# Optimization experiments

Measured on AMD Instinct MI355X. Metric: run time of the kernel, lower is better.

Reference implementation:

```python
import jax, jax.numpy as jnp
import numpy as np

B, P, S, D = 16, 512, 1024, 1024
H_FULL, H_LIGHT = 16, 8


def _mha(q, k, v, w_in, b_in, w_out, b_out, nh):
    # PyTorch nn.MultiheadAttention (batch_first=True), dropout=0 (eval).
    d = q.shape[-1]
    hd = d // nh
    wq, wk, wv = jnp.split(w_in, 3, axis=0)
    bq, bk, bv = jnp.split(b_in, 3, axis=0)

    def proj(x, w, b):
        return (x @ w.T + b).reshape(x.shape[0], x.shape[1], nh, hd)

    qh = proj(q, wq, bq)  # [B,Lq,H,hd]
    kh = proj(k, wk, bk)  # [B,Lk,H,hd]
    vh = proj(v, wv, bv)
    scale = 1.0 / jnp.sqrt(jnp.asarray(hd, q.dtype))
    scores = jnp.einsum('bqhd,bkhd->bhqk', qh, kh) * scale
    attn = jax.nn.softmax(scores, axis=-1)
    o = jnp.einsum('bhqk,bkhd->bqhd', attn, vh).reshape(q.shape[0], q.shape[1], d)
    out = o @ w_out.T + b_out
    return out, attn.mean(axis=1)  # avg weights over heads (torch default)


def _ln(x, g, b, eps=1e-5):
    mu = x.mean(-1, keepdims=True)
    var = ((x - mu) ** 2).mean(-1, keepdims=True)
    return (x - mu) / jnp.sqrt(var + eps) * g + b


def setup_inputs() -> dict:
    key = jax.random.key(0)
    ks = jax.random.split(key, 16)
    w = 0.02
    inp = {
        'proto': jax.random.normal(ks[0], (B, P, D), jnp.float32),
        'img_features': jax.random.normal(ks[1], (B, S, D), jnp.float32),
        'cross_w_in': jax.random.normal(ks[2], (3 * D, D), jnp.float32) * w,
        'cross_b_in': jnp.zeros((3 * D,), jnp.float32),
        'cross_w_out': jax.random.normal(ks[3], (D, D), jnp.float32) * w,
        'cross_b_out': jnp.zeros((D,), jnp.float32),
        'self_w_in': jax.random.normal(ks[4], (3 * D, D), jnp.float32) * w,
        'self_b_in': jnp.zeros((3 * D,), jnp.float32),
        'self_w_out': jax.random.normal(ks[5], (D, D), jnp.float32) * w,
        'self_b_out': jnp.zeros((D,), jnp.float32),
        'light_w_in': jax.random.normal(ks[6], (3 * D, D), jnp.float32) * w,
        'light_b_in': jnp.zeros((3 * D,), jnp.float32),
        'light_w_out': jax.random.normal(ks[7], (D, D), jnp.float32) * w,
        'light_b_out': jnp.zeros((D,), jnp.float32),
        'norm1_g': jnp.ones((D,), jnp.float32), 'norm1_b': jnp.zeros((D,), jnp.float32),
        'norm2_g': jnp.ones((D,), jnp.float32), 'norm2_b': jnp.zeros((D,), jnp.float32),
        'norm3_g': jnp.ones((D,), jnp.float32), 'norm3_b': jnp.zeros((D,), jnp.float32),
        'gate_w1': jax.random.normal(ks[8], (D, 3 * D), jnp.float32) * w,
        'gate_b1': jnp.zeros((D,), jnp.float32),
        'gate_w2': jax.random.normal(ks[9], (3, D), jnp.float32) * w,
        'gate_b2': jnp.zeros((3,), jnp.float32),
    }
    return inp


def reference(proto, img_features,
              cross_w_in, cross_b_in, cross_w_out, cross_b_out,
              self_w_in, self_b_in, self_w_out, self_b_out,
              light_w_in, light_b_in, light_w_out, light_b_out,
              norm1_g, norm1_b, norm2_g, norm2_b, norm3_g, norm3_b,
              gate_w1, gate_b1, gate_w2, gate_b2):
    cross_raw, attn_w = _mha(proto, img_features, img_features,
                             cross_w_in, cross_b_in, cross_w_out, cross_b_out, H_FULL)
    cross_out = _ln(proto + cross_raw, norm1_g, norm1_b)
    self_raw, _ = _mha(cross_out, cross_out, cross_out,
                       self_w_in, self_b_in, self_w_out, self_b_out, H_FULL)
    self_out = _ln(cross_out + self_raw, norm2_g, norm2_b)
    light_raw, _ = _mha(self_out, self_out, self_out,
                        light_w_in, light_b_in, light_w_out, light_b_out, H_LIGHT)
    light_out = _ln(self_out + light_raw, norm3_g, norm3_b)
    gate_in = jnp.concatenate([cross_out, self_out, light_out], axis=-1)  # [B,P,3D]
    h = jax.nn.gelu(gate_in @ gate_w1.T + gate_b1, approximate=False)
    gate_w = jax.nn.softmax(h @ gate_w2.T + gate_b2, axis=-1)  # [B,P,3]
    updated = (gate_w[..., 0:1] * cross_out
               + gate_w[..., 1:2] * self_out
               + gate_w[..., 2:3] * light_out)
    return updated, attn_w
```

## Files before the change

### kernel.cpp

```cpp
#include <hip/hip_runtime.h>
#include <hip/hip_bf16.h>

typedef __hip_bfloat16 bf16;
typedef __attribute__((ext_vector_type(8))) short short8;
typedef __attribute__((ext_vector_type(4))) float f32x4;

#define BD 16
#define PD 512
#define SD 1024
#define DD 1024

#define GLDS16(gp, lp)                                              \
  __builtin_amdgcn_global_load_lds(                                 \
      (const __attribute__((address_space(1))) void*)(gp),          \
      (__attribute__((address_space(3))) void*)(lp), 16, 0, 0)

__global__ __launch_bounds__(256) void f2b(const float* __restrict__ in,
                                           bf16* __restrict__ out, int n)
{
  int i = (blockIdx.x * 256 + threadIdx.x) * 4;
  if (i < n) {
    float4 v = *(const float4*)(in + i);
    out[i + 0] = __float2bfloat16(v.x);
    out[i + 1] = __float2bfloat16(v.y);
    out[i + 2] = __float2bfloat16(v.z);
    out[i + 3] = __float2bfloat16(v.w);
  }
}

__global__ __launch_bounds__(256) void gemm_nt(
    const bf16* __restrict__ A, int lda,
    const bf16* __restrict__ W, int ldw,
    const float* __restrict__ bias,
    bf16* __restrict__ C, int ldc,
    int K, int gelu)
{
  __shared__ bf16 As[3][128 * 32];
  __shared__ bf16 Bs[3][128 * 32];

  const int t = threadIdx.x;
  const int lane = t & 63, wv = t >> 6;
  const int m0 = blockIdx.y * 128;
  const int n0 = blockIdx.x * 128;
  const int rl = lane & 15, qd = lane >> 4;

  f32x4 acc[4][4];
  for (int i = 0; i < 4; i++)
    for (int j = 0; j < 4; j++)
      acc[i][j] = (f32x4){0.f, 0.f, 0.f, 0.f};

  const int scol = ((t & 3) ^ ((t >> 2) & 3)) * 8;
  const bf16* Ag = A + (size_t)(m0 + (t >> 2)) * lda + scol;
  const bf16* Wg = W + (size_t)(n0 + (t >> 2)) * ldw + scol;
  const size_t a_half = (size_t)64 * lda, w_half = (size_t)64 * ldw;
  const int lo = wv * 512;

  const int mw = (wv >> 1) * 64, nw = (wv & 1) * 64;
  const int slo = rl & 3;

  const int nt = K >> 5;

#define STAGE(buf, k0)                          \
  do {                                          \
    GLDS16(Ag + (k0), &As[buf][lo]);            \
    GLDS16(Ag + a_half + (k0), &As[buf][2048 + lo]); \
    GLDS16(Wg + (k0), &Bs[buf][lo]);            \
    GLDS16(Wg + w_half + (k0), &Bs[buf][2048 + lo]); \
  } while (0)

  STAGE(0, 0);
  STAGE(1, 32);

  int cur = 0, pf = 2;
  for (int tt = 0; tt < nt; ++tt) {
    if (tt + 1 < nt) asm volatile("s_waitcnt vmcnt(4)" ::: "memory");
    else             asm volatile("s_waitcnt vmcnt(0)" ::: "memory");
    __builtin_amdgcn_s_barrier();
    if (tt + 2 < nt) STAGE(pf, (tt + 2) * 32);

    const bf16* Ac = As[cur];
    const bf16* Bc = Bs[cur];
    short8 a[4], b[4];
#pragma unroll
    for (int i = 0; i < 4; i++)
      a[i] = *(const short8*)&Ac[(mw + i * 16 + rl) * 32 + (qd ^ slo) * 8];
#pragma unroll
    for (int j = 0; j < 4; j++)
      b[j] = *(const short8*)&Bc[(nw + j * 16 + rl) * 32 + (qd ^ slo) * 8];
#pragma unroll
    for (int i = 0; i < 4; i++)
#pragma unroll
      for (int j = 0; j < 4; j++)
        acc[i][j] = __builtin_amdgcn_mfma_f32_16x16x32_bf16(a[i], b[j], acc[i][j], 0, 0, 0);

    cur = (cur == 2) ? 0 : cur + 1;
    pf  = (pf == 2) ? 0 : pf + 1;
  }
#undef STAGE

  for (int i = 0; i < 4; i++) {
    const int row = m0 + mw + i * 16 + qd * 4;
    for (int j = 0; j < 4; j++) {
      const int col = n0 + nw + j * 16 + rl;
      const float bv = bias[col];
      for (int r = 0; r < 4; r++) {
        float v = acc[i][j][r] + bv;
        if (gelu) v = 0.5f * v * (1.0f + erff(v * 0.70710678118654752f));
        C[(size_t)(row + r) * ldc + col] = __float2bfloat16(v);
      }
    }
  }
}

__global__ __launch_bounds__(512, 2) void gemm_nt256(
    const bf16* __restrict__ A, int lda,
    const bf16* __restrict__ W, int ldw,
    const float* __restrict__ bias,
    bf16* __restrict__ C, int ldc,
    int K, int gelu)
{
  __shared__ bf16 As[2][256 * 64];
  __shared__ bf16 Bs[2][256 * 64];

  const int t = threadIdx.x;
  const int lane = t & 63, wv = t >> 6;
  const int rl = lane & 15, qd = lane >> 4;
  const int m0 = blockIdx.y * 256;
  const int n0 = blockIdx.x * 256;
  const int mw = (wv >> 2) * 128, nw = (wv & 3) * 64;

  f32x4 acc[8][4];
#pragma unroll
  for (int i = 0; i < 8; i++)
#pragma unroll
    for (int j = 0; j < 4; j++)
      acc[i][j] = (f32x4){0.f, 0.f, 0.f, 0.f};

  const int scol = ((t & 7) ^ ((t >> 3) & 7)) * 8;
  const bf16* Ag = A + (size_t)(m0 + (t >> 3)) * lda + scol;
  const bf16* Wg = W + (size_t)(n0 + (t >> 3)) * ldw + scol;

#define STAGE256(buf, k0)                                              \
  do {                                                                 \
    _Pragma("unroll")                                                  \
    for (int s = 0; s < 4; s++) {                                      \
      GLDS16(Ag + (size_t)(s * 64) * lda + (k0), &As[buf][s * 4096 + wv * 512]); \
      GLDS16(Wg + (size_t)(s * 64) * ldw + (k0), &Bs[buf][s * 4096 + wv * 512]); \
    }                                                                  \
  } while (0)

  const int nt = K >> 6;
  const int slo = rl & 7;

  STAGE256(0, 0);

  for (int tt = 0; tt < nt; ++tt) {
    if (tt + 1 < nt) {
      STAGE256((tt + 1) & 1, (tt + 1) * 64);
      asm volatile("s_waitcnt vmcnt(8)" ::: "memory");
    } else {
      asm volatile("s_waitcnt vmcnt(0)" ::: "memory");
    }
    __builtin_amdgcn_s_barrier();

    const bf16* Ac = As[tt & 1];
    const bf16* Bc = Bs[tt & 1];
#pragma unroll
    for (int kk = 0; kk < 2; ++kk) {
      const int cs = ((kk * 4 + qd) ^ slo) * 8;
      short8 a[8], b[4];
#pragma unroll
      for (int i = 0; i < 8; i++)
        a[i] = *(const short8*)&Ac[(mw + i * 16 + rl) * 64 + cs];
#pragma unroll
      for (int j = 0; j < 4; j++)
        b[j] = *(const short8*)&Bc[(nw + j * 16 + rl) * 64 + cs];
#pragma unroll
      for (int i = 0; i < 8; i++)
#pragma unroll
        for (int j = 0; j < 4; j++)
          acc[i][j] = __builtin_amdgcn_mfma_f32_16x16x32_bf16(a[i], b[j], acc[i][j], 0, 0, 0);
    }
    __builtin_amdgcn_s_barrier();
  }
#undef STAGE256

  for (int i = 0; i < 8; i++) {
    const int row = m0 + mw + i * 16 + qd * 4;
    for (int j = 0; j < 4; j++) {
      const int col = n0 + nw + j * 16 + rl;
      const float bv = bias[col];
      for (int r = 0; r < 4; r++) {
        float v = acc[i][j][r] + bv;
        if (gelu) v = 0.5f * v * (1.0f + erff(v * 0.70710678118654752f));
        C[(size_t)(row + r) * ldc + col] = __float2bfloat16(v);
      }
    }
  }
}

__global__ void transpose_v(const bf16* __restrict__ V, int ldv, int voff,
                            bf16* __restrict__ Vt, int L, int H, int hd)
{
  __shared__ float tile[32][33];
  const int bh = blockIdx.z;
  const int b = bh / H, h = bh % H;
  const int d0 = blockIdx.x * 32, s0 = blockIdx.y * 32;
  const int tx = threadIdx.x, ty = threadIdx.y;
  tile[ty][tx] = __bfloat162float(V[(size_t)(b * L + s0 + ty) * ldv + voff + h * hd + d0 + tx]);
  __syncthreads();
  Vt[(size_t)((b * H + h) * hd + d0 + ty) * L + s0 + tx] = __float2bfloat16(tile[tx][ty]);
}

template<int HD, bool STATS>
__global__ __launch_bounds__(256) void flash_attn(
    const bf16* __restrict__ Q, int ldq, int qoff,
    const bf16* __restrict__ Km, int ldk, int koff,
    const bf16* __restrict__ Vt,
    bf16* __restrict__ O, int ldo, int ooff,
    float* __restrict__ linv_out,
    int H, int Lq, int Lk, float scale)
{
  constexpr int KK = HD / 32;
  constexpr int NO = HD / 16;
  __shared__ __align__(16) __hip_bfloat16 pl[4][2][2][16][32];

  const int lane = threadIdx.x & 63, wv = threadIdx.x >> 6;
  const int rl = lane & 15, qd = lane >> 4;
  const int b = blockIdx.z, h = blockIdx.y;
  const int q0 = blockIdx.x * 128 + wv * 32;

  short8 qf[2][KK];
  for (int mt = 0; mt < 2; ++mt)
    for (int kk = 0; kk < KK; ++kk)
      qf[mt][kk] = *(const short8*)(Q + (size_t)(b * Lq + q0 + mt * 16 + rl) * ldq
                                      + qoff + h * HD + kk * 32 + qd * 8);

  const bf16* Kb = Km + (size_t)b * Lk * ldk + koff + h * HD + qd * 8;
  const bf16* Vb = Vt + (size_t)(b * H + h) * HD * Lk + qd * 8;

  float ls[2][4];
  for (int mt = 0; mt < 2; mt++)
    for (int r = 0; r < 4; r++) ls[mt][r] = 0.f;
  f32x4 oacc[2][NO];
  for (int mt = 0; mt < 2; mt++)
    for (int ni = 0; ni < NO; ni++) oacc[mt][ni] = (f32x4){0.f, 0.f, 0.f, 0.f};

  const int nS32 = Lk / 32;
  for (int i = 0; i < nS32; i++) {
    const int s0 = i * 32;
    for (int f = 0; f < 2; f++) {
      short8 kf[KK];
#pragma unroll
      for (int kk = 0; kk < KK; kk++)
        kf[kk] = *(const short8*)(Kb + (size_t)(s0 + f * 16 + rl) * ldk + kk * 32);
#pragma unroll
      for (int mt = 0; mt < 2; mt++) {
        f32x4 sc = (f32x4){0.f, 0.f, 0.f, 0.f};
#pragma unroll
        for (int kk = 0; kk < KK; kk++)
          sc = __builtin_amdgcn_mfma_f32_16x16x32_bf16(qf[mt][kk], kf[kk], sc, 0, 0, 0);
        for (int r = 0; r < 4; r++) {
          float p = __expf(sc[r] * scale);
          ls[mt][r] += p;
          pl[wv][i & 1][mt][qd * 4 + r][f * 16 + rl] = __float2bfloat16(p);
        }
      }
    }
    asm volatile("s_waitcnt lgkmcnt(0)" ::: "memory");
    short8 vf[NO];
#pragma unroll
    for (int ni = 0; ni < NO; ni++)
      vf[ni] = *(const short8*)(Vb + (size_t)(ni * 16 + rl) * Lk + s0);
#pragma unroll
    for (int mt = 0; mt < 2; mt++) {
      short8 pa = *(const short8*)&pl[wv][i & 1][mt][rl][qd * 8];
#pragma unroll
      for (int ni = 0; ni < NO; ni++)
        oacc[mt][ni] = __builtin_amdgcn_mfma_f32_16x16x32_bf16(pa, vf[ni], oacc[mt][ni], 0, 0, 0);
    }
  }

  float rinv[2][4];
  for (int mt = 0; mt < 2; mt++)
    for (int r = 0; r < 4; r++) {
      float v = ls[mt][r];
      for (int o = 1; o < 16; o <<= 1) v += __shfl_xor(v, o);
      rinv[mt][r] = 1.0f / v;
    }

  if (STATS) {
    if (rl == 0)
      for (int mt = 0; mt < 2; mt++)
        for (int r = 0; r < 4; r++)
          linv_out[((size_t)b * H + h) * Lq + q0 + mt * 16 + qd * 4 + r] = rinv[mt][r];
  }

  for (int mt = 0; mt < 2; mt++)
    for (int ni = 0; ni < NO; ni++)
      for (int r = 0; r < 4; r++)
        O[(size_t)(b * Lq + q0 + mt * 16 + qd * 4 + r) * ldo + ooff + h * HD + ni * 16 + rl]
            = __float2bfloat16(oacc[mt][ni][r] * rinv[mt][r]);
}

template<int HD>
__global__ __launch_bounds__(256) void probs_mean(
    const bf16* __restrict__ Q, int ldq, int qoff,
    const bf16* __restrict__ Km, int ldk, int koff,
    const float* __restrict__ linv, float* __restrict__ out_att,
    int H, int Lq, int Lk, float scale)
{
  constexpr int KK = HD / 32;
  const int lane = threadIdx.x & 63, wv = threadIdx.x >> 6;
  const int rl = lane & 15, qd = lane >> 4;
  const int b = blockIdx.z;
  const int q0 = blockIdx.x * 128 + wv * 32;
  const int s0 = blockIdx.y * 32;
  const float hs = 1.0f / 16.0f;

  f32x4 am[2][2];
  for (int mt = 0; mt < 2; mt++)
    for (int f = 0; f < 2; f++) am[mt][f] = (f32x4){0.f, 0.f, 0.f, 0.f};

  const bf16* Qb  = Q  + (size_t)(b * Lq + q0) * ldq + qoff + qd * 8;
  const bf16* Kb0 = Km + (size_t)(b * Lk + s0) * ldk + koff + qd * 8;
  const float* lb = linv + (size_t)b * H * Lq + q0 + qd * 4;

  for (int h = 0; h < H; h++) {
    short8 qf[2][KK], kf[2][KK];
#pragma unroll
    for (int mt = 0; mt < 2; mt++)
#pragma unroll
      for (int kk = 0; kk < KK; kk++)
        qf[mt][kk] = *(const short8*)(Qb + (size_t)(mt * 16 + rl) * ldq + h * HD + kk * 32);
#pragma unroll
    for (int f = 0; f < 2; f++)
#pragma unroll
      for (int kk = 0; kk < KK; kk++)
        kf[f][kk] = *(const short8*)(Kb0 + (size_t)(f * 16 + rl) * ldk + h * HD + kk * 32);
    float li[2][4];
#pragma unroll
    for (int mt = 0; mt < 2; mt++)
#pragma unroll
      for (int r = 0; r < 4; r++)
        li[mt][r] = lb[(size_t)h * Lq + mt * 16 + r];
#pragma unroll
    for (int mt = 0; mt < 2; mt++)
#pragma unroll
      for (int f = 0; f < 2; f++) {
        f32x4 sc = (f32x4){0.f, 0.f, 0.f, 0.f};
#pragma unroll
        for (int kk = 0; kk < KK; kk++)
          sc = __builtin_amdgcn_mfma_f32_16x16x32_bf16(qf[mt][kk], kf[f][kk], sc, 0, 0, 0);
#pragma unroll
        for (int r = 0; r < 4; r++)
          am[mt][f][r] += __expf(sc[r] * scale) * li[mt][r];
      }
  }

#pragma unroll
  for (int mt = 0; mt < 2; mt++)
#pragma unroll
    for (int f = 0; f < 2; f++)
#pragma unroll
      for (int r = 0; r < 4; r++)
        out_att[(size_t)(b * Lq + q0 + mt * 16 + qd * 4 + r) * Lk + s0 + f * 16 + rl]
            = am[mt][f][r] * hs;
}

template<bool XF32>
__global__ __launch_bounds__(256) void add_ln(
    const void* __restrict__ Xv, int ldx, int xoff,
    const bf16* __restrict__ Y,
    const float* __restrict__ g, const float* __restrict__ bb,
    bf16* __restrict__ out, int ldo, int ooff)
{
  const int row = blockIdx.x, t = threadIdx.x;
  const bf16* yr = Y + (size_t)row * 1024;
  float v[4], s = 0.f, s2 = 0.f;
  for (int i = 0; i < 4; i++) {
    int c = t * 4 + i;
    float xv;
    if (XF32) xv = ((const float*)Xv)[(size_t)row * ldx + xoff + c];
    else      xv = __bfloat162float(((const bf16*)Xv)[(size_t)row * ldx + xoff + c]);
    v[i] = xv + __bfloat162float(yr[c]);
    s += v[i]; s2 += v[i] * v[i];
  }
  __shared__ float red[2][4];
  for (int o = 32; o >= 1; o >>= 1) { s += __shfl_down(s, o); s2 += __shfl_down(s2, o); }
  const int wv = t >> 6, lane = t & 63;
  if (lane == 0) { red[0][wv] = s; red[1][wv] = s2; }
  __syncthreads();
  s  = red[0][0] + red[0][1] + red[0][2] + red[0][3];
  s2 = red[1][0] + red[1][1] + red[1][2] + red[1][3];
  const float mean = s * (1.0f / 1024.f);
  const float var = s2 * (1.0f / 1024.f) - mean * mean;
  const float rstd = rsqrtf(var + 1e-5f);
  for (int i = 0; i < 4; i++) {
    int c = t * 4 + i;
    float o = (v[i] - mean) * rstd * g[c] + bb[c];
    out[(size_t)row * ldo + ooff + c] = __float2bfloat16(o);
  }
}

__global__ __launch_bounds__(256) void gate_kernel(
    const bf16* __restrict__ Hb, const bf16* __restrict__ G,
    const float* __restrict__ w2, const float* __restrict__ b2,
    float* __restrict__ out)
{
  const int row = blockIdx.x, t = threadIdx.x;
  const bf16* hr = Hb + (size_t)row * 1024;
  float d0 = 0.f, d1 = 0.f, d2 = 0.f;
  for (int i = 0; i < 4; i++) {
    int c = t * 4 + i;
    float hv = __bfloat162float(hr[c]);
    d0 += hv * w2[c];
    d1 += hv * w2[1024 + c];
    d2 += hv * w2[2048 + c];
  }
  __shared__ float red[3][4];
  for (int o = 32; o >= 1; o >>= 1) {
    d0 += __shfl_down(d0, o); d1 += __shfl_down(d1, o); d2 += __shfl_down(d2, o);
  }
  const int wv = t >> 6, lane = t & 63;
  if (lane == 0) { red[0][wv] = d0; red[1][wv] = d1; red[2][wv] = d2; }
  __syncthreads();
  float l0 = red[0][0] + red[0][1] + red[0][2] + red[0][3] + b2[0];
  float l1 = red[1][0] + red[1][1] + red[1][2] + red[1][3] + b2[1];
  float l2 = red[2][0] + red[2][1] + red[2][2] + red[2][3] + b2[2];
  float mm = fmaxf(l0, fmaxf(l1, l2));
  float e0 = __expf(l0 - mm), e1 = __expf(l1 - mm), e2 = __expf(l2 - mm);
  float inv = 1.f / (e0 + e1 + e2);
  float g0 = e0 * inv, g1 = e1 * inv, g2 = e2 * inv;
  const bf16* gr = G + (size_t)row * 3072;
  for (int i = 0; i < 4; i++) {
    int c = t * 4 + i;
    float o = g0 * __bfloat162float(gr[c]) + g1 * __bfloat162float(gr[1024 + c])
            + g2 * __bfloat162float(gr[2048 + c]);
    out[(size_t)row * 1024 + c] = o;
  }
}

extern "C" void kernel_launch(void* const* d_in, const int* in_sizes, int n_in,
                              void* d_out, int out_size, void* d_ws, size_t ws_size,
                              hipStream_t stream)
{
  const float* proto = (const float*)d_in[0];
  const float* img   = (const float*)d_in[1];
  const float* c_wi  = (const float*)d_in[2];
  const float* c_bi  = (const float*)d_in[3];
  const float* c_wo  = (const float*)d_in[4];
  const float* c_bo  = (const float*)d_in[5];
  const float* s_wi  = (const float*)d_in[6];
  const float* s_bi  = (const float*)d_in[7];
  const float* s_wo  = (const float*)d_in[8];
  const float* s_bo  = (const float*)d_in[9];
  const float* l_wi  = (const float*)d_in[10];
  const float* l_bi  = (const float*)d_in[11];
  const float* l_wo  = (const float*)d_in[12];
  const float* l_bo  = (const float*)d_in[13];
  const float* n1g = (const float*)d_in[14]; const float* n1b = (const float*)d_in[15];
  const float* n2g = (const float*)d_in[16]; const float* n2b = (const float*)d_in[17];
  const float* n3g = (const float*)d_in[18]; const float* n3b = (const float*)d_in[19];
  const float* gw1 = (const float*)d_in[20]; const float* gb1 = (const float*)d_in[21];
  const float* gw2 = (const float*)d_in[22]; const float* gb2 = (const float*)d_in[23];

  float* out_upd = (float*)d_out;
  float* out_att = out_upd + (size_t)BD * PD * DD;

  char* ws = (char*)d_ws;
  bf16* WB = (bf16*)ws;
  bf16* w_cwi = WB + 0;
  bf16* w_cwo = WB + 3145728;
  bf16* w_swi = WB + 4194304;
  bf16* w_swo = WB + 7340032;
  bf16* w_lwi = WB + 8388608;
  bf16* w_lwo = WB + 11534336;
  bf16* w_gw1 = WB + 12582912;

  int bc = 16;
  while (bc > 1 && 31457280ull + (size_t)bc * 16777216ull > ws_size) bc >>= 1;

  char* pool = ws + 31457280;
  bf16*  Pb    = (bf16*)pool;
  bf16*  Ib    = (bf16*)(pool + (size_t)1048576 * bc);
  bf16*  G     = (bf16*)(pool + (size_t)3145728 * bc);
  bf16*  KVb   = (bf16*)(pool + (size_t)6291456 * bc);
  bf16*  Bq    = (bf16*)(pool + (size_t)8388608 * bc);
  bf16*  Vt    = (bf16*)(pool + (size_t)11534336 * bc);
  bf16*  Qc    = (bf16*)(pool + (size_t)13631488 * bc);
  bf16*  AO    = (bf16*)(pool + (size_t)14680064 * bc);
  bf16*  OP    = (bf16*)(pool + (size_t)15728640 * bc);
  float* linvb = (float*)(pool + (size_t)15728640 * bc);

  const dim3 blk(256);
  const dim3 blk512(512);

  f2b<<<dim3(3072), blk, 0, stream>>>(c_wi, w_cwi, 3145728);
  f2b<<<dim3(1024), blk, 0, stream>>>(c_wo, w_cwo, 1048576);
  f2b<<<dim3(3072), blk, 0, stream>>>(s_wi, w_swi, 3145728);
  f2b<<<dim3(1024), blk, 0, stream>>>(s_wo, w_swo, 1048576);
  f2b<<<dim3(3072), blk, 0, stream>>>(l_wi, w_lwi, 3145728);
  f2b<<<dim3(1024), blk, 0, stream>>>(l_wo, w_lwo, 1048576);
  f2b<<<dim3(3072), blk, 0, stream>>>(gw1, w_gw1, 3145728);

  for (int b0 = 0; b0 < BD; b0 += bc) {
    const float* proto_c = proto + (size_t)b0 * PD * DD;
    const float* img_c   = img + (size_t)b0 * SD * DD;
    float* out_upd_c = out_upd + (size_t)b0 * PD * DD;
    float* out_att_c = out_att + (size_t)b0 * PD * SD;
    const int MP = bc * PD;
    const int MS = bc * SD;

    f2b<<<dim3(MP), blk, 0, stream>>>(proto_c, Pb, MP * DD);
    f2b<<<dim3(MS), blk, 0, stream>>>(img_c, Ib, MS * DD);

    gemm_nt<<<dim3(8, MP / 128), blk, 0, stream>>>(Pb, 1024, w_cwi, 1024, c_bi,
                                                   Qc, 1024, 1024, 0);
    gemm_nt256<<<dim3(8, MS / 256), blk512, 0, stream>>>(
        Ib, 1024, w_cwi + (size_t)1024 * 1024, 1024, c_bi + 1024, KVb, 2048, 1024, 0);
    transpose_v<<<dim3(2, 32, bc * 16), dim3(32, 32), 0, stream>>>(KVb, 2048, 1024, Vt, 1024, 16, 64);
    flash_attn<64, true><<<dim3(4, 16, bc), blk, 0, stream>>>(
        Qc, 1024, 0, KVb, 2048, 0, Vt, AO, 1024, 0, linvb, 16, PD, SD, 0.125f);
    probs_mean<64><<<dim3(4, SD / 32, bc), blk, 0, stream>>>(
        Qc, 1024, 0, KVb, 2048, 0, linvb, out_att_c, 16, PD, SD, 0.125f);
    gemm_nt<<<dim3(8, MP / 128), blk, 0, stream>>>(AO, 1024, w_cwo, 1024, c_bo, OP, 1024, 1024, 0);
    add_ln<true><<<dim3(MP), blk, 0, stream>>>(proto_c, 1024, 0, OP, n1g, n1b, G, 3072, 0);

    gemm_nt256<<<dim3(12, MP / 256), blk512, 0, stream>>>(
        G, 3072, w_swi, 1024, s_bi, Bq, 3072, 1024, 0);
    transpose_v<<<dim3(2, 16, bc * 16), dim3(32, 32), 0, stream>>>(Bq, 3072, 2048, Vt, 512, 16, 64);
    flash_attn<64, false><<<dim3(4, 16, bc), blk, 0, stream>>>(
        Bq, 3072, 0, Bq, 3072, 1024, Vt, AO, 1024, 0, nullptr, 16, PD, PD, 0.125f);
    gemm_nt<<<dim3(8, MP / 128), blk, 0, stream>>>(AO, 1024, w_swo, 1024, s_bo, OP, 1024, 1024, 0);
    add_ln<false><<<dim3(MP), blk, 0, stream>>>(G, 3072, 0, OP, n2g, n2b, G, 3072, 1024);

    gemm_nt256<<<dim3(12, MP / 256), blk512, 0, stream>>>(
        G + 1024, 3072, w_lwi, 1024, l_bi, Bq, 3072, 1024, 0);
    transpose_v<<<dim3(4, 16, bc * 8), dim3(32, 32), 0, stream>>>(Bq, 3072, 2048, Vt, 512, 8, 128);
    flash_attn<128, false><<<dim3(4, 8, bc), blk, 0, stream>>>(
        Bq, 3072, 0, Bq, 3072, 1024, Vt, AO, 1024, 0, nullptr, 8, PD, PD,
        0.08838834764831845f);
    gemm_nt<<<dim3(8, MP / 128), blk, 0, stream>>>(AO, 1024, w_lwo, 1024, l_bo, OP, 1024, 1024, 0);
    add_ln<false><<<dim3(MP), blk, 0, stream>>>(G, 3072, 1024, OP, n3g, n3b, G, 3072, 2048);

    gemm_nt256<<<dim3(4, MP / 256), blk512, 0, stream>>>(
        G, 3072, w_gw1, 3072, gb1, Qc, 1024, 3072, 1);
    gate_kernel<<<dim3(MP), blk, 0, stream>>>(Qc, G, gw2, gb2, out_upd_c);
  }
}
```

Before: 1.507 ms.

## Split 256-tile GEMM into four interleaved load/MFMA phases per K step

```diff
diff --git a/kernel.cpp b/kernel.cpp
--- a/kernel.cpp
+++ b/kernel.cpp
@@ -112,7 +112,7 @@
   }
 }
 
-__global__ __launch_bounds__(512, 2) void gemm_nt256(
+__global__ __launch_bounds__(512, 2) void gemm8p(
     const bf16* __restrict__ A, int lda,
     const bf16* __restrict__ W, int ldw,
     const float* __restrict__ bias,
@@ -125,66 +125,78 @@
   const int t = threadIdx.x;
   const int lane = t & 63, wv = t >> 6;
   const int rl = lane & 15, qd = lane >> 4;
-  const int m0 = blockIdx.y * 256;
-  const int n0 = blockIdx.x * 256;
+  const int m0 = blockIdx.y * 256, n0 = blockIdx.x * 256;
+  const int aw = (wv >> 2) * 64;
+  const int bw = (wv & 3) * 32;
+  const int slo = rl & 7;
+
+  f32x4 acc[8][4];
+#pragma unroll
+  for (int i = 0; i < 8; i++)
+#pragma unroll
+    for (int j = 0; j < 4; j++) acc[i][j] = (f32x4){0.f, 0.f, 0.f, 0.f};
+
+  const int lr = lane >> 3;
+  const int scol = ((lane & 7) ^ lr) * 8;
+  const bf16* Ag = A + (size_t)(m0 + wv * 8 + lr) * lda + scol;
+  const bf16* Wg = W + (size_t)(n0 + (wv >> 2) * 64 + (wv & 3) * 8 + lr) * ldw + scol;
+  const int ldsw = wv * 512;
+
+#define ST_ALO(bf_, k0_) { GLDS16(Ag + (k0_), &As[bf_][ldsw]);                     \
+                           GLDS16(Ag + (size_t)128 * lda + (k0_), &As[bf_][4096 + ldsw]); }
+#define ST_AHI(bf_, k0_) { GLDS16(Ag + (size_t)64 * lda + (k0_), &As[bf_][8192 + ldsw]); \
+                           GLDS16(Ag + (size_t)192 * lda + (k0_), &As[bf_][12288 + ldsw]); }
+#define ST_BLO(bf_, k0_) { GLDS16(Wg + (k0_), &Bs[bf_][ldsw]);                     \
+                           GLDS16(Wg + (size_t)128 * ldw + (k0_), &Bs[bf_][4096 + ldsw]); }
+#define ST_BHI(bf_, k0_) { GLDS16(Wg + (size_t)32 * ldw + (k0_), &Bs[bf_][8192 + ldsw]); \
+                           GLDS16(Wg + (size_t)160 * ldw + (k0_), &Bs[bf_][12288 + ldsw]); }
+
+#define PHASE(rb_, mh_, nh_, STG)                                                   \
+  {                                                                                 \
+    short8 a0[4][2], b0[2][2];                                                      \
+    const bf16* Ab_ = &As[rb_][(size_t)((mh_) * 128 + aw) * 64];                    \
+    const bf16* Bb_ = &Bs[rb_][(size_t)((nh_) * 128 + bw) * 64];                    \
+    _Pragma("unroll") for (int i2 = 0; i2 < 4; i2++)                                \
+      _Pragma("unroll") for (int kk = 0; kk < 2; kk++)                              \
+        a0[i2][kk] = *(const short8*)&Ab_[(i2 * 16 + rl) * 64 + ((kk * 4 + qd) ^ slo) * 8]; \
+    _Pragma("unroll") for (int j2 = 0; j2 < 2; j2++)                                \
+      _Pragma("unroll") for (int kk = 0; kk < 2; kk++)                              \
+        b0[j2][kk] = *(const short8*)&Bb_[(j2 * 16 + rl) * 64 + ((kk * 4 + qd) ^ slo) * 8]; \
+    STG;                                                                            \
+    asm volatile("s_waitcnt vmcnt(4)" ::: "memory");                                \
+    __builtin_amdgcn_s_barrier();                                                   \
+    __builtin_amdgcn_s_setprio(1);                                                  \
+    _Pragma("unroll") for (int i2 = 0; i2 < 4; i2++)                                \
+      _Pragma("unroll") for (int j2 = 0; j2 < 2; j2++)                              \
+        _Pragma("unroll") for (int kk = 0; kk < 2; kk++)                            \
+          acc[(mh_) * 4 + i2][(nh_) * 2 + j2] = __builtin_amdgcn_mfma_f32_16x16x32_bf16( \
+              a0[i2][kk], b0[j2][kk], acc[(mh_) * 4 + i2][(nh_) * 2 + j2], 0, 0, 0); \
+    __builtin_amdgcn_s_setprio(0);                                                  \
+    __builtin_amdgcn_s_barrier();                                                   \
+  }
+
+  const int nt = K >> 6;
+
+  ST_ALO(0, 0); ST_BLO(0, 0); ST_AHI(0, 0); ST_BHI(0, 0);
+  asm volatile("s_waitcnt vmcnt(4)" ::: "memory");
+  __builtin_amdgcn_s_barrier();
+
+  for (int tt = 0; tt < nt; ++tt) {
+    const int rb = tt & 1, sb = rb ^ 1;
+    const int kn = (tt + 1) << 6;
+    const bool st = (tt + 1) < nt;
+    PHASE(rb, 0, 0, if (st) ST_ALO(sb, kn));
+    PHASE(rb, 1, 0, if (st) ST_BLO(sb, kn));
+    PHASE(rb, 0, 1, if (st) ST_AHI(sb, kn));
+    PHASE(rb, 1, 1, if (st) ST_BHI(sb, kn));
+  }
+#undef PHASE
+#undef ST_ALO
+#undef ST_AHI
+#undef ST_BLO
+#undef ST_BHI
+
   const int mw = (wv >> 2) * 128, nw = (wv & 3) * 64;
-
-  f32x4 acc[8][4];
-#pragma unroll
-  for (int i = 0; i < 8; i++)
-#pragma unroll
-    for (int j = 0; j < 4; j++)
-      acc[i][j] = (f32x4){0.f, 0.f, 0.f, 0.f};
-
-  const int scol = ((t & 7) ^ ((t >> 3) & 7)) * 8;
-  const bf16* Ag = A + (size_t)(m0 + (t >> 3)) * lda + scol;
-  const bf16* Wg = W + (size_t)(n0 + (t >> 3)) * ldw + scol;
-
-#define STAGE256(buf, k0)                                              \
-  do {                                                                 \
-    _Pragma("unroll")                                                  \
-    for (int s = 0; s < 4; s++) {                                      \
-      GLDS16(Ag + (size_t)(s * 64) * lda + (k0), &As[buf][s * 4096 + wv * 512]); \
-      GLDS16(Wg + (size_t)(s * 64) * ldw + (k0), &Bs[buf][s * 4096 + wv * 512]); \
-    }                                                                  \
-  } while (0)
-
-  const int nt = K >> 6;
-  const int slo = rl & 7;
-
-  STAGE256(0, 0);
-
-  for (int tt = 0; tt < nt; ++tt) {
-    if (tt + 1 < nt) {
-      STAGE256((tt + 1) & 1, (tt + 1) * 64);
-      asm volatile("s_waitcnt vmcnt(8)" ::: "memory");
-    } else {
-      asm volatile("s_waitcnt vmcnt(0)" ::: "memory");
-    }
-    __builtin_amdgcn_s_barrier();
-
-    const bf16* Ac = As[tt & 1];
-    const bf16* Bc = Bs[tt & 1];
-#pragma unroll
-    for (int kk = 0; kk < 2; ++kk) {
-      const int cs = ((kk * 4 + qd) ^ slo) * 8;
-      short8 a[8], b[4];
-#pragma unroll
-      for (int i = 0; i < 8; i++)
-        a[i] = *(const short8*)&Ac[(mw + i * 16 + rl) * 64 + cs];
-#pragma unroll
-      for (int j = 0; j < 4; j++)
-        b[j] = *(const short8*)&Bc[(nw + j * 16 + rl) * 64 + cs];
-#pragma unroll
-      for (int i = 0; i < 8; i++)
-#pragma unroll
-        for (int j = 0; j < 4; j++)
-          acc[i][j] = __builtin_amdgcn_mfma_f32_16x16x32_bf16(a[i], b[j], acc[i][j], 0, 0, 0);
-    }
-    __builtin_amdgcn_s_barrier();
-  }
-#undef STAGE256
-
   for (int i = 0; i < 8; i++) {
     const int row = m0 + mw + i * 16 + qd * 4;
     for (int j = 0; j < 4; j++) {
@@ -517,7 +529,7 @@
 
     gemm_nt<<<dim3(8, MP / 128), blk, 0, stream>>>(Pb, 1024, w_cwi, 1024, c_bi,
                                                    Qc, 1024, 1024, 0);
-    gemm_nt256<<<dim3(8, MS / 256), blk512, 0, stream>>>(
+    gemm8p<<<dim3(8, MS / 256), blk512, 0, stream>>>(
         Ib, 1024, w_cwi + (size_t)1024 * 1024, 1024, c_bi + 1024, KVb, 2048, 1024, 0);
     transpose_v<<<dim3(2, 32, bc * 16), dim3(32, 32), 0, stream>>>(KVb, 2048, 1024, Vt, 1024, 16, 64);
     flash_attn<64, true><<<dim3(4, 16, bc), blk, 0, stream>>>(
@@ -527,7 +539,7 @@
     gemm_nt<<<dim3(8, MP / 128), blk, 0, stream>>>(AO, 1024, w_cwo, 1024, c_bo, OP, 1024, 1024, 0);
     add_ln<true><<<dim3(MP), blk, 0, stream>>>(proto_c, 1024, 0, OP, n1g, n1b, G, 3072, 0);
 
-    gemm_nt256<<<dim3(12, MP / 256), blk512, 0, stream>>>(
+    gemm8p<<<dim3(12, MP / 256), blk512, 0, stream>>>(
         G, 3072, w_swi, 1024, s_bi, Bq, 3072, 1024, 0);
     transpose_v<<<dim3(2, 16, bc * 16), dim3(32, 32), 0, stream>>>(Bq, 3072, 2048, Vt, 512, 16, 64);
     flash_attn<64, false><<<dim3(4, 16, bc), blk, 0, stream>>>(
@@ -535,7 +547,7 @@
     gemm_nt<<<dim3(8, MP / 128), blk, 0, stream>>>(AO, 1024, w_swo, 1024, s_bo, OP, 1024, 1024, 0);
     add_ln<false><<<dim3(MP), blk, 0, stream>>>(G, 3072, 0, OP, n2g, n2b, G, 3072, 1024);
 
-    gemm_nt256<<<dim3(12, MP / 256), blk512, 0, stream>>>(
+    gemm8p<<<dim3(12, MP / 256), blk512, 0, stream>>>(
         G + 1024, 3072, w_lwi, 1024, l_bi, Bq, 3072, 1024, 0);
     transpose_v<<<dim3(4, 16, bc * 8), dim3(32, 32), 0, stream>>>(Bq, 3072, 2048, Vt, 512, 8, 128);
     flash_attn<128, false><<<dim3(4, 8, bc), blk, 0, stream>>>(
@@ -544,8 +556,7 @@
     gemm_nt<<<dim3(8, MP / 128), blk, 0, stream>>>(AO, 1024, w_lwo, 1024, l_bo, OP, 1024, 1024, 0);
     add_ln<false><<<dim3(MP), blk, 0, stream>>>(G, 3072, 1024, OP, n3g, n3b, G, 3072, 2048);
 
-    gemm_nt256<<<dim3(4, MP / 256), blk512, 0, stream>>>(
-        G, 3072, w_gw1, 3072, gb1, Qc, 1024, 3072, 1);
+    gemm_nt<<<dim3(8, MP / 128), blk, 0, stream>>>(G, 3072, w_gw1, 3072, gb1, Qc, 1024, 3072, 1);
     gate_kernel<<<dim3(MP), blk, 0, stream>>>(Qc, G, gw2, gb2, out_upd_c);
   }
 }
```

Measured after the change: 1.435 ms. 4.8% less time.
